# Performance work log

Hardware: AMD Instinct MI355X
Metric: run time of the kernel (lower is better)

## Reference

```python
import jax, jax.numpy as jnp
import numpy as np

B, N, D = 2, 2048, 768
H = 12
DH = D // H
SCALE = DH ** -0.5


def setup_inputs() -> dict:
    key = jax.random.key(0)
    k1, k2, k3 = jax.random.split(key, 3)
    x = jax.random.normal(k1, (B, N, D), dtype=jnp.float32)
    w_qkv = jax.random.normal(k2, (D, 3 * D), dtype=jnp.float32) * (D ** -0.5)
    b_qkv = jnp.zeros((3 * D,), dtype=jnp.float32)
    w_proj = jax.random.normal(k3, (D, D), dtype=jnp.float32) * (D ** -0.5)
    b_proj = jnp.zeros((D,), dtype=jnp.float32)
    return {"x": x, "w_qkv": w_qkv, "b_qkv": b_qkv, "w_proj": w_proj, "b_proj": b_proj}


def reference(x, w_qkv, b_qkv, w_proj, b_proj):
    b, n, d = x.shape
    # qkv: (B, n, 3, H, DH) -> (3, B, H, n, DH)
    qkv = (x @ w_qkv + b_qkv).reshape(b, n, 3, H, DH).transpose(2, 0, 3, 1, 4)
    q, k, v = qkv[0], qkv[1], qkv[2]
    # naive full attention matrix (B, H, n, n)
    attn = jnp.einsum('bhqd,bhkd->bhqk', q, k) * SCALE
    attn = jax.nn.softmax(attn, axis=-1)
    out = jnp.einsum('bhqk,bhkd->bhqd', attn, v)  # (B, H, n, DH)
    out = out.transpose(0, 2, 1, 3).reshape(b, n, d)
    return out @ w_proj + b_proj
```

## Files before the change

kernel.cpp:

```cpp
#include <hip/hip_runtime.h>


#define CB 2
#define CN 2048
#define CD 768
#define CH 12
#define CDH 64
#define CEXPSCALE 0.18033688f

typedef __bf16 bf16x8 __attribute__((ext_vector_type(8)));
typedef float f32x4 __attribute__((ext_vector_type(4)));
typedef unsigned short u16x8 __attribute__((ext_vector_type(8)));

static __device__ __forceinline__ unsigned short f2bf(float f) {
  union { float f; unsigned u; } v; v.f = f;
  unsigned r = v.u + 0x7fffu + ((v.u >> 16) & 1u);
  return (unsigned short)(r >> 16);
}

static __device__ __forceinline__ void gld_lds16(const unsigned short* g, unsigned short* lds_base) {
  __builtin_amdgcn_global_load_lds(
      (const __attribute__((address_space(1))) unsigned int*)g,
      (__attribute__((address_space(3))) unsigned int*)(unsigned int)(unsigned long long)lds_base,
      16, 0, 0);
}

__global__ __launch_bounds__(256) void prep(const float* __restrict__ x,
                                            unsigned short* __restrict__ xb,
                                            const float* __restrict__ w_qkv,
                                            unsigned short* __restrict__ wqkv_t,
                                            const float* __restrict__ w_proj,
                                            unsigned short* __restrict__ wproj_t) {
  __shared__ __align__(16) unsigned short t[64][72];
  const int bid = blockIdx.x, tid = threadIdx.x;
#pragma unroll
  for (int it = 0; it < 2; ++it) {
    size_t i = ((size_t)(bid * 2 + it) * 256 + tid) * 8;
    f32x4 a = *(const f32x4*)&x[i];
    f32x4 b = *(const f32x4*)&x[i + 4];
    u16x8 o;
#pragma unroll
    for (int j = 0; j < 4; ++j) { o[j] = f2bf(a[j]); o[4 + j] = f2bf(b[j]); }
    *(u16x8*)&xb[i] = o;
  }
  if (bid >= 576) return;
  const float* src; unsigned short* dst; int R, C, c0, r0;
  if (bid < 432) { src = w_qkv; dst = wqkv_t; R = 768; C = 2304; c0 = (bid % 36) * 64; r0 = (bid / 36) * 64; }
  else { int u = bid - 432; src = w_proj; dst = wproj_t; R = 768; C = 768; c0 = (u % 12) * 64; r0 = (u / 12) * 64; }
#pragma unroll
  for (int i = 0; i < 4; ++i) {
    int c = tid + i * 256;
    int row = c >> 4, cc = (c & 15) * 4;
    f32x4 v = *(const f32x4*)&src[(size_t)(r0 + row) * C + c0 + cc];
#pragma unroll
    for (int j = 0; j < 4; ++j) t[row][cc + j] = f2bf(v[j]);
  }
  __syncthreads();
#pragma unroll
  for (int i = 0; i < 2; ++i) {
    int c = tid + i * 256;
    int drow = c >> 3, rc = (c & 7) * 8;
    u16x8 v;
#pragma unroll
    for (int j = 0; j < 8; ++j) v[j] = t[rc + j][drow];
    *(u16x8*)&dst[(size_t)(c0 + drow) * R + r0 + rc] = v;
  }
}

extern __shared__ __align__(16) unsigned short smem[];
__global__ __launch_bounds__(256) void gemm128(const unsigned short* __restrict__ A,
                                               const unsigned short* __restrict__ Bt,
                                               const float* __restrict__ bias,
                                               int M, int N, int K, int mode,
                                               unsigned short* __restrict__ o0,
                                               unsigned short* __restrict__ o1,
                                               unsigned short* __restrict__ o2,
                                               float* __restrict__ outF) {
  unsigned short* As = smem;
  unsigned short* Bs = smem + 128 * 32;
  unsigned short* Ct = smem;
  const int tid = threadIdx.x;
  const int w = tid >> 6, lane = tid & 63, quad = lane >> 4, lc = lane & 15;
  const int wm = (w >> 1) * 64, wn = (w & 1) * 64;
  const int row0 = blockIdx.y * 128, col0 = blockIdx.x * 128;
  f32x4 acc[4][4] = {};

  const int rl = lane >> 2, cl = lane & 3;
  const int gc = cl ^ ((rl >> 1) & 3);
  const int rsw = (lc >> 1) & 3;

  for (int k0 = 0; k0 < K; k0 += 32) {
#pragma unroll
    for (int j = 0; j < 2; ++j) {
      int r = w * 32 + j * 16 + rl;
      gld_lds16(&A[(size_t)(row0 + r) * K + k0 + gc * 8], &As[(w * 32 + j * 16) * 32]);
      gld_lds16(&Bt[(size_t)(col0 + r) * K + k0 + gc * 8], &Bs[(w * 32 + j * 16) * 32]);
    }
    __syncthreads();
    bf16x8 af[4], bfv[4];
#pragma unroll
    for (int mt = 0; mt < 4; ++mt)
      af[mt] = *(const bf16x8*)&As[(wm + mt * 16 + lc) * 32 + (quad ^ rsw) * 8];
#pragma unroll
    for (int nt = 0; nt < 4; ++nt)
      bfv[nt] = *(const bf16x8*)&Bs[(wn + nt * 16 + lc) * 32 + (quad ^ rsw) * 8];
#pragma unroll
    for (int mt = 0; mt < 4; ++mt)
#pragma unroll
      for (int nt = 0; nt < 4; ++nt)
        acc[mt][nt] = __builtin_amdgcn_mfma_f32_16x16x32_bf16(af[mt], bfv[nt], acc[mt][nt], 0, 0, 0);
    __syncthreads();
  }

  if (mode == 0 && col0 >= 1536) {
#pragma unroll
    for (int mt = 0; mt < 4; ++mt) {
#pragma unroll
      for (int nt = 0; nt < 4; ++nt) {
        int jl = wn + nt * 16 + lc;
        int il0 = wm + mt * 16 + quad * 4;
        float bj = bias[col0 + jl];
        unsigned short a0 = f2bf(acc[mt][nt][0] + bj);
        unsigned short a1 = f2bf(acc[mt][nt][1] + bj);
        unsigned short a2 = f2bf(acc[mt][nt][2] + bj);
        unsigned short a3 = f2bf(acc[mt][nt][3] + bj);
        uint2 dd;
        dd.x = (unsigned)a0 | ((unsigned)a1 << 16);
        dd.y = (unsigned)a2 | ((unsigned)a3 << 16);
        *(uint2*)&Ct[jl * 136 + il0] = dd;
      }
    }
    __syncthreads();
    const int b = row0 >> 11, n0 = row0 & 2047;
#pragma unroll
    for (int i = 0; i < 8; ++i) {
      int c = tid + i * 256;
      int jl = c >> 4, cc = (c & 15) * 8;
      u16x8 v = *(const u16x8*)&Ct[jl * 136 + cc];
      int jcol = col0 - 1536 + jl;
      int h = jcol >> 6, d = jcol & 63;
      size_t gr = ((size_t)(b * CH + h) * CDH + d);
      *(u16x8*)&o2[gr * CN + n0 + cc] = v;
    }
  } else {
#pragma unroll
    for (int mt = 0; mt < 4; ++mt) {
#pragma unroll
      for (int nt = 0; nt < 4; ++nt) {
#pragma unroll
        for (int r = 0; r < 4; ++r) {
          int i = row0 + wm + mt * 16 + quad * 4 + r;
          int j = col0 + wn + nt * 16 + lc;
          float v = acc[mt][nt][r] + bias[j];
          if (mode == 0) {
            int b = i >> 11, n = i & 2047;
            int sec = (j >= 768) ? 1 : 0;
            int within = j - sec * 768;
            int h = within >> 6, d = within & 63;
            int bh = b * CH + h;
            if (sec == 0) o0[((size_t)bh * CN + n) * CDH + d] = f2bf(v * CEXPSCALE);
            else          o1[((size_t)bh * CN + n) * CDH + d] = f2bf(v);
          } else {
            outF[(size_t)i * N + j] = v;
          }
        }
      }
    }
  }
}

__global__ __launch_bounds__(256, 3) void attn64(const unsigned short* __restrict__ Q,
                                                 const unsigned short* __restrict__ K,
                                                 const unsigned short* __restrict__ Vt,
                                                 unsigned short* __restrict__ O) {
  __shared__ __align__(16) unsigned short Kls[2][64 * 64];
  __shared__ __align__(16) unsigned short Vls[2][64 * 64];
  __shared__ __align__(16) unsigned short P[4][16][88];
  const int bh = blockIdx.x, qt = blockIdx.y;
  const int tid = threadIdx.x;
  const int w = tid >> 6, lane = tid & 63, quad = lane >> 4, lc = lane & 15;
  const unsigned short* Qb = Q + (size_t)bh * CN * CDH;
  const unsigned short* Kb = K + (size_t)bh * CN * CDH;
  const unsigned short* Vb = Vt + (size_t)bh * CDH * CN;
  const int q0 = qt * 64 + w * 16;

  const int sr = lane >> 3, sc = lane & 7;
  const int sg = sc ^ sr;
  const int ksw = lc & 7;
  const int c0r = quad ^ ksw;
  const int c1r = c0r ^ 4;

  bf16x8 qf0 = *(const bf16x8*)&Qb[(size_t)(q0 + lc) * CDH + quad * 8];
  bf16x8 qf1 = *(const bf16x8*)&Qb[(size_t)(q0 + lc) * CDH + 32 + quad * 8];

  f32x4 o[4] = {};
  float rs = 0.f;

#pragma unroll
  for (int j2 = 0; j2 < 2; ++j2) {
    int j = w * 2 + j2;
    int r = j * 8 + sr;
    gld_lds16(&Kb[(size_t)r * CDH + sg * 8], &Kls[0][j * 8 * 64]);
    gld_lds16(&Vb[(size_t)r * CN + 0 + sg * 8], &Vls[0][j * 8 * 64]);
  }

  for (int kt = 0; kt < CN / 64; ++kt) {
    const int bb = kt & 1;
    __syncthreads();
    if (kt + 1 < CN / 64) {
      const int kn = (kt + 1) * 64;
#pragma unroll
      for (int j2 = 0; j2 < 2; ++j2) {
        int j = w * 2 + j2;
        int r = j * 8 + sr;
        gld_lds16(&Kb[(size_t)(kn + r) * CDH + sg * 8], &Kls[bb ^ 1][j * 8 * 64]);
        gld_lds16(&Vb[(size_t)r * CN + kn + sg * 8], &Vls[bb ^ 1][j * 8 * 64]);
      }
    }
#pragma unroll
    for (int t = 0; t < 4; ++t) {
      bf16x8 kf0 = *(const bf16x8*)&Kls[bb][(t * 16 + lc) * 64 + c0r * 8];
      bf16x8 kf1 = *(const bf16x8*)&Kls[bb][(t * 16 + lc) * 64 + c1r * 8];
      f32x4 z = {0.f, 0.f, 0.f, 0.f};
      z = __builtin_amdgcn_mfma_f32_16x16x32_bf16(kf0, qf0, z, 0, 0, 0);
      z = __builtin_amdgcn_mfma_f32_16x16x32_bf16(kf1, qf1, z, 0, 0, 0);
      float p0 = exp2f(z[0]);
      float p1 = exp2f(z[1]);
      float p2 = exp2f(z[2]);
      float p3 = exp2f(z[3]);
      rs += (p0 + p1) + (p2 + p3);
      unsigned d0 = __builtin_amdgcn_perm(__float_as_uint(p1), __float_as_uint(p0), 0x07060302u);
      unsigned d1 = __builtin_amdgcn_perm(__float_as_uint(p3), __float_as_uint(p2), 0x07060302u);
      uint2 dd; dd.x = d0; dd.y = d1;
      *(uint2*)&P[w][lc][t * 16 + quad * 4] = dd;
    }
    asm volatile("s_waitcnt lgkmcnt(0)" ::: "memory");
    bf16x8 pf0 = *(const bf16x8*)&P[w][lc][quad * 8];
    bf16x8 pf1 = *(const bf16x8*)&P[w][lc][32 + quad * 8];
#pragma unroll
    for (int dt = 0; dt < 4; ++dt) {
      bf16x8 vf0 = *(const bf16x8*)&Vls[bb][(dt * 16 + lc) * 64 + c0r * 8];
      bf16x8 vf1 = *(const bf16x8*)&Vls[bb][(dt * 16 + lc) * 64 + c1r * 8];
      o[dt] = __builtin_amdgcn_mfma_f32_16x16x32_bf16(pf0, vf0, o[dt], 0, 0, 0);
      o[dt] = __builtin_amdgcn_mfma_f32_16x16x32_bf16(pf1, vf1, o[dt], 0, 0, 0);
    }
  }

  rs += __shfl_xor(rs, 16, 64);
  rs += __shfl_xor(rs, 32, 64);
  const int b = bh / CH, h = bh - b * CH;
#pragma unroll
  for (int r = 0; r < 4; ++r) {
    float lr = __shfl(rs, quad * 4 + r, 64);
    float inv = 1.0f / lr;
#pragma unroll
    for (int dt = 0; dt < 4; ++dt) {
      int i = b * CN + q0 + quad * 4 + r;
      int j = h * CDH + dt * 16 + lc;
      O[(size_t)i * CD + j] = f2bf(o[dt][r] * inv);
    }
  }
}

extern "C" void kernel_launch(void* const* d_in, const int* in_sizes, int n_in,
                              void* d_out, int out_size, void* d_ws, size_t ws_size,
                              hipStream_t stream) {
  const float* x      = (const float*)d_in[0];
  const float* w_qkv  = (const float*)d_in[1];
  const float* b_qkv  = (const float*)d_in[2];
  const float* w_proj = (const float*)d_in[3];
  const float* b_proj = (const float*)d_in[4];
  float* out = (float*)d_out;
  unsigned short* ws = (unsigned short*)d_ws;

  unsigned short* xb      = ws;
  unsigned short* wqkv_t  = xb + (size_t)4096 * 768;
  unsigned short* wproj_t = wqkv_t + (size_t)2304 * 768;
  unsigned short* Qs  = wproj_t + (size_t)768 * 768;
  unsigned short* Ks  = Qs  + (size_t)CB * CH * CN * CDH;
  unsigned short* Vts = Ks  + (size_t)CB * CH * CN * CDH;
  unsigned short* AO  = Vts + (size_t)CB * CH * CN * CDH;

  const size_t smem_qkv  = (size_t)(128 * 136) * 2;
  const size_t smem_proj = (size_t)(128 * 32 * 2) * 2;

  prep<<<768, 256, 0, stream>>>(x, xb, w_qkv, wqkv_t, w_proj, wproj_t);
  gemm128<<<dim3(2304 / 128, 4096 / 128), 256, smem_qkv, stream>>>(
      xb, wqkv_t, b_qkv, 4096, 2304, 768, 0, Qs, Ks, Vts, nullptr);
  attn64<<<dim3(CB * CH, CN / 64), 256, 0, stream>>>(Qs, Ks, Vts, AO);
  gemm128<<<dim3(768 / 128, 4096 / 128), 256, smem_proj, stream>>>(
      AO, wproj_t, b_proj, 4096, 768, 768, 1, nullptr, nullptr, nullptr, out);
}
```

Before: 192.2 us.

## Double-buffer GEMM LDS tiles and shrink tiles to raise block count

New measurement: 169.6 us. -11.8%, faster.

```diff
diff --git a/kernel.cpp b/kernel.cpp
--- a/kernel.cpp
+++ b/kernel.cpp
@@ -68,55 +68,66 @@
 }
 
 extern __shared__ __align__(16) unsigned short smem[];
-__global__ __launch_bounds__(256) void gemm128(const unsigned short* __restrict__ A,
-                                               const unsigned short* __restrict__ Bt,
-                                               const float* __restrict__ bias,
-                                               int M, int N, int K, int mode,
-                                               unsigned short* __restrict__ o0,
-                                               unsigned short* __restrict__ o1,
-                                               unsigned short* __restrict__ o2,
-                                               float* __restrict__ outF) {
+
+template <int TM, int TN>
+__global__ __launch_bounds__(256, 4) void gemm_db(const unsigned short* __restrict__ A,
+                                                  const unsigned short* __restrict__ Bt,
+                                                  const float* __restrict__ bias,
+                                                  int M, int N, int K, int mode,
+                                                  unsigned short* __restrict__ o0,
+                                                  unsigned short* __restrict__ o1,
+                                                  unsigned short* __restrict__ o2,
+                                                  float* __restrict__ outF) {
+  constexpr int NT = TN / 32;
   unsigned short* As = smem;
-  unsigned short* Bs = smem + 128 * 32;
+  unsigned short* Bs = smem + 2 * TM * 32;
   unsigned short* Ct = smem;
   const int tid = threadIdx.x;
   const int w = tid >> 6, lane = tid & 63, quad = lane >> 4, lc = lane & 15;
-  const int wm = (w >> 1) * 64, wn = (w & 1) * 64;
-  const int row0 = blockIdx.y * 128, col0 = blockIdx.x * 128;
-  f32x4 acc[4][4] = {};
+  const int wm = (w >> 1) * 32, wn = (w & 1) * (TN / 2);
+  const int row0 = blockIdx.y * TM, col0 = blockIdx.x * TN;
+  f32x4 acc[2][NT] = {};
 
   const int rl = lane >> 2, cl = lane & 3;
   const int gc = cl ^ ((rl >> 1) & 3);
   const int rsw = (lc >> 1) & 3;
-
-  for (int k0 = 0; k0 < K; k0 += 32) {
-#pragma unroll
-    for (int j = 0; j < 2; ++j) {
-      int r = w * 32 + j * 16 + rl;
-      gld_lds16(&A[(size_t)(row0 + r) * K + k0 + gc * 8], &As[(w * 32 + j * 16) * 32]);
-      gld_lds16(&Bt[(size_t)(col0 + r) * K + k0 + gc * 8], &Bs[(w * 32 + j * 16) * 32]);
-    }
+  const int nk = K / 32;
+
+  auto stage = [&](int kt, int buf) {
+    const int k0 = kt * 32;
+    gld_lds16(&A[(size_t)(row0 + w * 16 + rl) * K + k0 + gc * 8],
+              &As[buf * (TM * 32) + (w * 16) * 32]);
+#pragma unroll
+    for (int jb = 0; jb < TN / 64; ++jb)
+      gld_lds16(&Bt[(size_t)(col0 + w * (TN / 4) + jb * 16 + rl) * K + k0 + gc * 8],
+                &Bs[buf * (TN * 32) + (w * (TN / 4) + jb * 16) * 32]);
+  };
+
+  stage(0, 0);
+  for (int kt = 0; kt < nk; ++kt) {
+    const int bb = kt & 1;
     __syncthreads();
-    bf16x8 af[4], bfv[4];
-#pragma unroll
-    for (int mt = 0; mt < 4; ++mt)
-      af[mt] = *(const bf16x8*)&As[(wm + mt * 16 + lc) * 32 + (quad ^ rsw) * 8];
-#pragma unroll
-    for (int nt = 0; nt < 4; ++nt)
-      bfv[nt] = *(const bf16x8*)&Bs[(wn + nt * 16 + lc) * 32 + (quad ^ rsw) * 8];
-#pragma unroll
-    for (int mt = 0; mt < 4; ++mt)
-#pragma unroll
-      for (int nt = 0; nt < 4; ++nt)
+    if (kt + 1 < nk) stage(kt + 1, bb ^ 1);
+    bf16x8 af[2], bfv[NT];
+#pragma unroll
+    for (int mt = 0; mt < 2; ++mt)
+      af[mt] = *(const bf16x8*)&As[bb * (TM * 32) + (wm + mt * 16 + lc) * 32 + (quad ^ rsw) * 8];
+#pragma unroll
+    for (int nt = 0; nt < NT; ++nt)
+      bfv[nt] = *(const bf16x8*)&Bs[bb * (TN * 32) + (wn + nt * 16 + lc) * 32 + (quad ^ rsw) * 8];
+#pragma unroll
+    for (int mt = 0; mt < 2; ++mt)
+#pragma unroll
+      for (int nt = 0; nt < NT; ++nt)
         acc[mt][nt] = __builtin_amdgcn_mfma_f32_16x16x32_bf16(af[mt], bfv[nt], acc[mt][nt], 0, 0, 0);
+  }
+
+  if (mode == 0 && col0 >= 1536) {
     __syncthreads();
-  }
-
-  if (mode == 0 && col0 >= 1536) {
-#pragma unroll
-    for (int mt = 0; mt < 4; ++mt) {
-#pragma unroll
-      for (int nt = 0; nt < 4; ++nt) {
+#pragma unroll
+    for (int mt = 0; mt < 2; ++mt) {
+#pragma unroll
+      for (int nt = 0; nt < NT; ++nt) {
         int jl = wn + nt * 16 + lc;
         int il0 = wm + mt * 16 + quad * 4;
         float bj = bias[col0 + jl];
@@ -127,16 +138,17 @@
         uint2 dd;
         dd.x = (unsigned)a0 | ((unsigned)a1 << 16);
         dd.y = (unsigned)a2 | ((unsigned)a3 << 16);
-        *(uint2*)&Ct[jl * 136 + il0] = dd;
+        *(uint2*)&Ct[jl * (TM + 8) + il0] = dd;
       }
     }
     __syncthreads();
     const int b = row0 >> 11, n0 = row0 & 2047;
-#pragma unroll
-    for (int i = 0; i < 8; ++i) {
+    constexpr int CPR = TM / 8;
+#pragma unroll
+    for (int i = 0; i < (TN * CPR) / 256; ++i) {
       int c = tid + i * 256;
-      int jl = c >> 4, cc = (c & 15) * 8;
-      u16x8 v = *(const u16x8*)&Ct[jl * 136 + cc];
+      int jl = c / CPR, cc = (c % CPR) * 8;
+      u16x8 v = *(const u16x8*)&Ct[jl * (TM + 8) + cc];
       int jcol = col0 - 1536 + jl;
       int h = jcol >> 6, d = jcol & 63;
       size_t gr = ((size_t)(b * CH + h) * CDH + d);
@@ -144,9 +156,9 @@
     }
   } else {
 #pragma unroll
-    for (int mt = 0; mt < 4; ++mt) {
-#pragma unroll
-      for (int nt = 0; nt < 4; ++nt) {
+    for (int mt = 0; mt < 2; ++mt) {
+#pragma unroll
+      for (int nt = 0; nt < NT; ++nt) {
 #pragma unroll
         for (int r = 0; r < 4; ++r) {
           int i = row0 + wm + mt * 16 + quad * 4 + r;
@@ -281,13 +293,13 @@
   unsigned short* Vts = Ks  + (size_t)CB * CH * CN * CDH;
   unsigned short* AO  = Vts + (size_t)CB * CH * CN * CDH;
 
-  const size_t smem_qkv  = (size_t)(128 * 136) * 2;
-  const size_t smem_proj = (size_t)(128 * 32 * 2) * 2;
+  const size_t smem_qkv  = (size_t)2 * (64 + 128) * 32 * 2;
+  const size_t smem_proj = (size_t)2 * (64 + 64) * 32 * 2;
 
   prep<<<768, 256, 0, stream>>>(x, xb, w_qkv, wqkv_t, w_proj, wproj_t);
-  gemm128<<<dim3(2304 / 128, 4096 / 128), 256, smem_qkv, stream>>>(
+  gemm_db<64, 128><<<dim3(2304 / 128, 4096 / 64), 256, smem_qkv, stream>>>(
       xb, wqkv_t, b_qkv, 4096, 2304, 768, 0, Qs, Ks, Vts, nullptr);
   attn64<<<dim3(CB * CH, CN / 64), 256, 0, stream>>>(Qs, Ks, Vts, AO);
-  gemm128<<<dim3(768 / 128, 4096 / 128), 256, smem_proj, stream>>>(
+  gemm_db<64, 64><<<dim3(768 / 64, 4096 / 64), 256, smem_proj, stream>>>(
       AO, wproj_t, b_proj, 4096, 768, 768, 1, nullptr, nullptr, nullptr, out);
 }
```
